# Kernel tuning notes

Measured on AMD Instinct MI355X. Metric: run time of the kernel, lower is better.

Reference implementation:

```python
import jax, jax.numpy as jnp
import numpy as np

H = 12        # heads
D = 768       # d_model
DK = D // H   # per-head dim
B, S = 1, 4096


def setup_inputs() -> dict:
    key = jax.random.key(0)
    ks = jax.random.split(key, 8)
    scale = 1.0 / np.sqrt(D)
    return {
        "q": jax.random.normal(ks[0], (B, S, D), jnp.float32),
        "k": jax.random.normal(ks[1], (B, S, D), jnp.float32),
        "v": jax.random.normal(ks[2], (B, S, D), jnp.float32),
        "Wq": jax.random.normal(ks[3], (D, D), jnp.float32) * scale,
        "bq": jnp.zeros((D,), jnp.float32),
        "Wk": jax.random.normal(ks[4], (D, D), jnp.float32) * scale,
        "bk": jnp.zeros((D,), jnp.float32),
        "Wv": jax.random.normal(ks[5], (D, D), jnp.float32) * scale,
        "bv": jnp.zeros((D,), jnp.float32),
        "Wo": jax.random.normal(ks[6], (D, D), jnp.float32) * scale,
        "bo": jnp.zeros((D,), jnp.float32),
    }


def reference(q, k, v, Wq, bq, Wk, bk, Wv, bv, Wo, bo):
    bs, sq, _ = q.shape
    sk = k.shape[1]
    # projections, then split heads: (b, h, s, dk)
    qh = (q @ Wq + bq).reshape(bs, sq, H, DK).transpose(0, 2, 1, 3)
    kh = (k @ Wk + bk).reshape(bs, sk, H, DK).transpose(0, 2, 1, 3)
    vh = (v @ Wv + bv).reshape(bs, sk, H, DK).transpose(0, 2, 1, 3)
    # scaled dot-product attention (mask=None, dropout inactive)
    scores = jnp.einsum("bhqd,bhkd->bhqk", qh, kh) / jnp.sqrt(jnp.float32(DK))
    attn = jax.nn.softmax(scores, axis=-1)
    ctx = jnp.einsum("bhqk,bhkd->bhqd", attn, vh)
    concat = ctx.transpose(0, 2, 1, 3).reshape(bs, sq, D)
    return concat @ Wo + bo
```

## Files before the change

kernel.cpp:

```cpp
#include <hip/hip_runtime.h>
#include <hip/hip_bf16.h>


constexpr int S_LEN = 4096;
constexpr int D_MODEL = 768;
constexpr int N_HEADS = 12;
constexpr int D_HEAD = 64;
constexpr int SEG = 2;
constexpr int SEG_LEN = S_LEN / SEG;
constexpr int NITER = SEG_LEN / 64;

#define QSCALE 0.180336880111120f

typedef _Float16 f16;
typedef __attribute__((ext_vector_type(8))) _Float16 f16x8;
typedef __attribute__((ext_vector_type(4))) _Float16 f16x4;
typedef __attribute__((ext_vector_type(4))) float f32x4;

__global__ __launch_bounds__(256) void prep_kernel(
    const float* __restrict__ q, const float* __restrict__ k,
    const float* __restrict__ v, f16* __restrict__ qh,
    f16* __restrict__ kh, f16* __restrict__ vh,
    const float* __restrict__ W0, const float* __restrict__ W1,
    const float* __restrict__ W2, const float* __restrict__ W3,
    f16* __restrict__ WtBase)
{
    __shared__ float T[64][65];
    int bid = blockIdx.x;
    const int t = threadIdx.x;
    if (bid < 4608) {
        int g = bid / 1536, r = bid % 1536;
        const float* x = (g == 0) ? q : (g == 1) ? k : v;
        f16* y = (g == 0) ? qh : (g == 1) ? kh : vh;
        int i = (r * 256 + t) * 8;
        float4 a = *(const float4*)&x[i];
        float4 b = *(const float4*)&x[i + 4];
        f16x8 h = { (f16)a.x, (f16)a.y, (f16)a.z, (f16)a.w,
                    (f16)b.x, (f16)b.y, (f16)b.z, (f16)b.w };
        *(f16x8*)&y[i] = h;
        return;
    }
    bid -= 4608;
    int g = bid / 144, r = bid % 144;
    const float* W = (g == 0) ? W0 : (g == 1) ? W1 : (g == 2) ? W2 : W3;
    f16* Wt = WtBase + (size_t)g * D_MODEL * D_MODEL;
    const int r0 = (r / 12) * 64;
    const int c0 = (r % 12) * 64;
    #pragma unroll
    for (int i = 0; i < 16; ++i) {
        int e = t + 256 * i; int rr = e >> 6, cc = e & 63;
        T[rr][cc] = W[(size_t)(r0 + rr) * D_MODEL + c0 + cc];
    }
    __syncthreads();
    #pragma unroll
    for (int i = 0; i < 16; ++i) {
        int e = t + 256 * i; int rr = e >> 6, cc = e & 63;
        Wt[(size_t)(c0 + rr) * D_MODEL + r0 + cc] = (f16)T[cc][rr];
    }
}

#define GSTR 72

__device__ __forceinline__ void gemm128_core(
    const f16* __restrict__ A, const f16* __restrict__ B,
    f16* As, f16* Bs, int K, int row0, int col0, int t, f32x4 acc[4][4])
{
    const int w = t >> 6, l = t & 63, quad = l >> 4, l15 = l & 15;
    const int wm = (w & 1) * 64, wn = (w >> 1) * 64;

    f16x8 pa[4], pb[4];
    #pragma unroll
    for (int i = 0; i < 4; ++i) {
        int idx = i * 256 + t;
        int r = idx >> 3, c = (idx & 7) * 8;
        pa[i] = *(const f16x8*)&A[(size_t)(row0 + r) * K + c];
        pb[i] = *(const f16x8*)&B[(size_t)(col0 + r) * K + c];
    }

    for (int k0 = 0; k0 < K; k0 += 64) {
        __syncthreads();
        #pragma unroll
        for (int i = 0; i < 4; ++i) {
            int idx = i * 256 + t;
            int r = idx >> 3, c = (idx & 7) * 8;
            *(f16x8*)&As[r * GSTR + c] = pa[i];
            *(f16x8*)&Bs[r * GSTR + c] = pb[i];
        }
        __syncthreads();

        int kn = k0 + 64;
        if (kn < K) {
            #pragma unroll
            for (int i = 0; i < 4; ++i) {
                int idx = i * 256 + t;
                int r = idx >> 3, c = (idx & 7) * 8;
                pa[i] = *(const f16x8*)&A[(size_t)(row0 + r) * K + kn + c];
                pb[i] = *(const f16x8*)&B[(size_t)(col0 + r) * K + kn + c];
            }
        }

        #pragma unroll
        for (int kc = 0; kc < 2; ++kc) {
            f16x8 af[4], bf[4];
            #pragma unroll
            for (int mt = 0; mt < 4; ++mt)
                af[mt] = *(f16x8*)&As[(wm + mt * 16 + l15) * GSTR + kc * 32 + quad * 8];
            #pragma unroll
            for (int nt = 0; nt < 4; ++nt)
                bf[nt] = *(f16x8*)&Bs[(wn + nt * 16 + l15) * GSTR + kc * 32 + quad * 8];
            #pragma unroll
            for (int mt = 0; mt < 4; ++mt)
                #pragma unroll
                for (int nt = 0; nt < 4; ++nt)
                    acc[mt][nt] = __builtin_amdgcn_mfma_f32_16x16x32_f16(
                        af[mt], bf[nt], acc[mt][nt], 0, 0, 0);
        }
    }
}

__global__ __launch_bounds__(256) void qkv_gemm_kernel(
    const f16* __restrict__ qh, const f16* __restrict__ kh,
    const f16* __restrict__ vh, const f16* __restrict__ WtBase,
    const float* __restrict__ bq, const float* __restrict__ bk,
    const float* __restrict__ bv,
    f16* __restrict__ Qp, f16* __restrict__ Kp, f16* __restrict__ Vpt)
{
    __shared__ f16 As[128 * GSTR];
    __shared__ f16 Bs[128 * GSTR];
    const size_t DD = (size_t)D_MODEL * D_MODEL;
    int bid = blockIdx.x;
    int g = bid / 192, r = bid % 192;

    const f16 *A, *B; const float* bias; f16* Y;
    int N; bool biasRow; float scale;
    int row0, col0;
    if (g == 0) {
        A = qh; B = WtBase; bias = bq; Y = Qp;
        N = D_MODEL; biasRow = false; scale = QSCALE;
        row0 = (r / 6) * 128; col0 = (r % 6) * 128;
    } else if (g == 1) {
        A = kh; B = WtBase + DD; bias = bk; Y = Kp;
        N = D_MODEL; biasRow = false; scale = 1.0f;
        row0 = (r / 6) * 128; col0 = (r % 6) * 128;
    } else {
        A = WtBase + 2 * DD; B = vh; bias = bv; Y = Vpt;
        N = S_LEN; biasRow = true; scale = 1.0f;
        row0 = (r / 32) * 128; col0 = (r % 32) * 128;
    }

    f32x4 acc[4][4];
    #pragma unroll
    for (int i = 0; i < 4; ++i)
        #pragma unroll
        for (int j = 0; j < 4; ++j) acc[i][j] = (f32x4){0.f, 0.f, 0.f, 0.f};

    const int t = threadIdx.x;
    gemm128_core(A, B, As, Bs, D_MODEL, row0, col0, t, acc);

    const int w = t >> 6, l = t & 63, quad = l >> 4, l15 = l & 15;
    const int wm = (w & 1) * 64, wn = (w >> 1) * 64;
    #pragma unroll
    for (int mt = 0; mt < 4; ++mt) {
        #pragma unroll
        for (int nt = 0; nt < 4; ++nt) {
            int col = col0 + wn + nt * 16 + l15;
            #pragma unroll
            for (int reg = 0; reg < 4; ++reg) {
                int row = row0 + wm + mt * 16 + quad * 4 + reg;
                float b = biasRow ? bias[row] : bias[col];
                Y[(size_t)row * N + col] = (f16)((acc[mt][nt][reg] + b) * scale);
            }
        }
    }
}

#define LSTR 72

__global__ __launch_bounds__(256, 4) void flash_attn_part_kernel(
    const f16* __restrict__ Q, const f16* __restrict__ K,
    const f16* __restrict__ Vg, f16* __restrict__ Opart,
    float* __restrict__ lsum)
{
    __shared__ f16 Ks[2][64 * LSTR];
    __shared__ f16 Vt[2][64 * LSTR];

    const int t    = threadIdx.x;
    const int w    = t >> 6;
    const int l    = t & 63;
    const int quad = l >> 4;
    const int l15  = l & 15;
    const int h    = blockIdx.y;
    const int q0   = blockIdx.x * 128;
    const int seg  = blockIdx.z;
    const int c0   = h * D_HEAD;
    const size_t SD = (size_t)S_LEN * D_MODEL;

    const int sr = t >> 3;
    const int sc = (t & 7) * 8;

    f16x8 qa[2][2];
    #pragma unroll
    for (int qt = 0; qt < 2; ++qt) {
        const f16* qrow = Q + (size_t)(q0 + w * 32 + qt * 16 + l15) * D_MODEL + c0;
        qa[qt][0] = *(const f16x8*)&qrow[quad * 8];
        qa[qt][1] = *(const f16x8*)&qrow[32 + quad * 8];
    }

    f32x4 ctx[2][4];
    float lAcc[2] = {0.f, 0.f};
    #pragma unroll
    for (int qt = 0; qt < 2; ++qt)
        #pragma unroll
        for (int i = 0; i < 4; ++i) ctx[qt][i] = (f32x4){0.f, 0.f, 0.f, 0.f};

    const int kt0 = seg * SEG_LEN;

    f16x8 kreg[2], vreg[2];
    #pragma unroll
    for (int i = 0; i < 2; ++i) {
        int r = i * 32 + sr;
        kreg[i] = *(const f16x8*)&K[(size_t)(kt0 + r) * D_MODEL + c0 + sc];
        vreg[i] = *(const f16x8*)&Vg[(size_t)(c0 + r) * S_LEN + kt0 + sc];
    }
    #pragma unroll
    for (int i = 0; i < 2; ++i) {
        int r = i * 32 + sr;
        *(f16x8*)&Ks[0][r * LSTR + sc] = kreg[i];
        *(f16x8*)&Vt[0][r * LSTR + sc] = vreg[i];
    }
    __syncthreads();
    #pragma unroll
    for (int i = 0; i < 2; ++i) {
        int r = i * 32 + sr;
        kreg[i] = *(const f16x8*)&K[(size_t)(kt0 + 64 + r) * D_MODEL + c0 + sc];
        vreg[i] = *(const f16x8*)&Vg[(size_t)(c0 + r) * S_LEN + kt0 + 64 + sc];
    }

    for (int it = 0; it < NITER; ++it) {
        const int buf = it & 1;
        const f16* ks = Ks[buf];
        const f16* vt = Vt[buf];

        f16x4 pfrag[2][4];
        #pragma unroll
        for (int nt = 0; nt < 4; ++nt) {
            f16x8 kb0 = *(const f16x8*)&ks[(nt * 16 + l15) * LSTR + quad * 8];
            f16x8 kb1 = *(const f16x8*)&ks[(nt * 16 + l15) * LSTR + 32 + quad * 8];
            #pragma unroll
            for (int qt = 0; qt < 2; ++qt) {
                f32x4 z = (f32x4){0.f, 0.f, 0.f, 0.f};
                z = __builtin_amdgcn_mfma_f32_16x16x32_f16(kb0, qa[qt][0], z, 0, 0, 0);
                z = __builtin_amdgcn_mfma_f32_16x16x32_f16(kb1, qa[qt][1], z, 0, 0, 0);
                float p0 = __builtin_amdgcn_exp2f(z[0]);
                float p1 = __builtin_amdgcn_exp2f(z[1]);
                float p2 = __builtin_amdgcn_exp2f(z[2]);
                float p3 = __builtin_amdgcn_exp2f(z[3]);
                lAcc[qt] += (p0 + p1) + (p2 + p3);
                pfrag[qt][nt] = (f16x4){ (f16)p0, (f16)p1, (f16)p2, (f16)p3 };
            }
        }
        #pragma unroll
        for (int mt = 0; mt < 4; ++mt) {
            #pragma unroll
            for (int nt = 0; nt < 4; ++nt) {
                f16x4 va = *(const f16x4*)&vt[(mt * 16 + l15) * LSTR + nt * 16 + quad * 4];
                #pragma unroll
                for (int qt = 0; qt < 2; ++qt)
                    ctx[qt][mt] = __builtin_amdgcn_mfma_f32_16x16x16f16(
                        va, pfrag[qt][nt], ctx[qt][mt], 0, 0, 0);
            }
        }

        if (it + 1 < NITER) {
            #pragma unroll
            for (int i = 0; i < 2; ++i) {
                int r = i * 32 + sr;
                *(f16x8*)&Ks[1 - buf][r * LSTR + sc] = kreg[i];
                *(f16x8*)&Vt[1 - buf][r * LSTR + sc] = vreg[i];
            }
        }
        __syncthreads();

        if (it + 2 < NITER) {
            int ktn = kt0 + (it + 2) * 64;
            #pragma unroll
            for (int i = 0; i < 2; ++i) {
                int r = i * 32 + sr;
                kreg[i] = *(const f16x8*)&K[(size_t)(ktn + r) * D_MODEL + c0 + sc];
                vreg[i] = *(const f16x8*)&Vg[(size_t)(c0 + r) * S_LEN + ktn + sc];
            }
        }
    }

    #pragma unroll
    for (int qt = 0; qt < 2; ++qt) {
        int qrow = q0 + w * 32 + qt * 16 + l15;
        #pragma unroll
        for (int mt = 0; mt < 4; ++mt) {
            f16x4 ov = { (f16)ctx[qt][mt][0], (f16)ctx[qt][mt][1],
                         (f16)ctx[qt][mt][2], (f16)ctx[qt][mt][3] };
            *(f16x4*)&Opart[(size_t)seg * SD + (size_t)qrow * D_MODEL
                            + c0 + mt * 16 + quad * 4] = ov;
        }
        float s = lAcc[qt];
        s += __shfl_xor(s, 16);
        s += __shfl_xor(s, 32);
        if (quad == 0)
            lsum[((size_t)seg * N_HEADS + h) * S_LEN + qrow] = s;
    }
}

__global__ __launch_bounds__(256) void combine_kernel(
    const f16* __restrict__ Opart, const float* __restrict__ lsum,
    f16* __restrict__ Ctx)
{
    const size_t SD = (size_t)S_LEN * D_MODEL;
    int tid = blockIdx.x * 256 + threadIdx.x;
    int idx = tid * 8;
    int row = idx / D_MODEL;
    int c   = idx % D_MODEL;
    int h   = c >> 6;
    float l0 = lsum[(size_t)h * S_LEN + row];
    float l1 = lsum[((size_t)N_HEADS + h) * S_LEN + row];
    float inv = 1.0f / (l0 + l1);
    f16x8 o0 = *(const f16x8*)&Opart[(size_t)row * D_MODEL + c];
    f16x8 o1 = *(const f16x8*)&Opart[SD + (size_t)row * D_MODEL + c];
    f16x8 r;
    #pragma unroll
    for (int j = 0; j < 8; ++j)
        r[j] = (f16)(((float)o0[j] + (float)o1[j]) * inv);
    *(f16x8*)&Ctx[(size_t)row * D_MODEL + c] = r;
}

__global__ __launch_bounds__(256) void oproj_kernel(
    const f16* __restrict__ Ctx, const f16* __restrict__ Wto,
    const float* __restrict__ bo, float* __restrict__ out)
{
    __shared__ f16 As[128 * GSTR];
    __shared__ f16 Bs[128 * GSTR];
    int bid = blockIdx.x;
    int row0 = (bid / 6) * 128, col0 = (bid % 6) * 128;

    f32x4 acc[4][4];
    #pragma unroll
    for (int i = 0; i < 4; ++i)
        #pragma unroll
        for (int j = 0; j < 4; ++j) acc[i][j] = (f32x4){0.f, 0.f, 0.f, 0.f};

    const int t = threadIdx.x;
    gemm128_core(Ctx, Wto, As, Bs, D_MODEL, row0, col0, t, acc);

    const int w = t >> 6, l = t & 63, quad = l >> 4, l15 = l & 15;
    const int wm = (w & 1) * 64, wn = (w >> 1) * 64;
    #pragma unroll
    for (int mt = 0; mt < 4; ++mt) {
        #pragma unroll
        for (int nt = 0; nt < 4; ++nt) {
            int col = col0 + wn + nt * 16 + l15;
            float b = bo[col];
            #pragma unroll
            for (int reg = 0; reg < 4; ++reg) {
                int row = row0 + wm + mt * 16 + quad * 4 + reg;
                out[(size_t)row * D_MODEL + col] = acc[mt][nt][reg] + b;
            }
        }
    }
}

extern "C" void kernel_launch(void* const* d_in, const int* in_sizes, int n_in,
                              void* d_out, int out_size, void* d_ws, size_t ws_size,
                              hipStream_t stream)
{
    const float* q  = (const float*)d_in[0];
    const float* k  = (const float*)d_in[1];
    const float* v  = (const float*)d_in[2];
    const float* Wq = (const float*)d_in[3];
    const float* bq = (const float*)d_in[4];
    const float* Wk = (const float*)d_in[5];
    const float* bk = (const float*)d_in[6];
    const float* Wv = (const float*)d_in[7];
    const float* bv = (const float*)d_in[8];
    const float* Wo = (const float*)d_in[9];
    const float* bo = (const float*)d_in[10];
    float* out = (float*)d_out;

    const size_t SD = (size_t)S_LEN * D_MODEL;
    const size_t DD = (size_t)D_MODEL * D_MODEL;
    f16* base   = (f16*)d_ws;
    f16* WtBase = base;
    f16* Wto    = WtBase + 3 * DD;
    f16* Qp     = base + 4 * DD;
    f16* Kp     = Qp + SD;
    f16* Vpt    = Kp + SD;
    f16* qh     = Vpt + SD;
    f16* kh     = qh + SD;
    f16* vh     = kh + SD;
    f16* Opart  = qh;
    f16* Ctx    = qh + 2 * SD;
    float* lsum = (float*)(base + 4 * DD + 6 * SD);

    prep_kernel<<<3 * 1536 + 4 * 144, 256, 0, stream>>>(
        q, k, v, qh, kh, vh, Wq, Wk, Wv, Wo, WtBase);

    qkv_gemm_kernel<<<3 * 192, 256, 0, stream>>>(
        qh, kh, vh, WtBase, bq, bk, bv, Qp, Kp, Vpt);

    dim3 gAttn(S_LEN / 128, N_HEADS, SEG);
    flash_attn_part_kernel<<<gAttn, 256, 0, stream>>>(Qp, Kp, Vpt, Opart, lsum);

    combine_kernel<<<1536, 256, 0, stream>>>(Opart, lsum, Ctx);

    oproj_kernel<<<192, 256, 0, stream>>>(Ctx, Wto, bo, out);
}
```

Before: 222.0 us.

## Use 512-thread attention blocks with one 16-row query tile per wave

Raises the flash-attention block from 4 to 8 waves, with each wave handling one 16-row query tile instead of two. Each thread now loads a single K/V staging row rather than two. This cuts per-thread register use and aims to raise occupancy (launch bounds 512,6). In exchange, each K/V tile in LDS is reused by fewer query rows per wave and there are more waves per barrier, which lowers MFMA work per LDS read and adds sync cost.

Measured after the change: 238.5 us. 1.07x slower.

```diff
diff --git a/kernel.cpp b/kernel.cpp
--- a/kernel.cpp
+++ b/kernel.cpp
@@ -176,7 +176,7 @@
 
 #define LSTR 72
 
-__global__ __launch_bounds__(256, 4) void flash_attn_part_kernel(
+__global__ __launch_bounds__(512, 6) void flash_attn_part_kernel(
     const f16* __restrict__ Q, const f16* __restrict__ K,
     const f16* __restrict__ Vg, f16* __restrict__ Opart,
     float* __restrict__ lsum)
@@ -198,115 +198,83 @@
     const int sr = t >> 3;
     const int sc = (t & 7) * 8;
 
-    f16x8 qa[2][2];
-    #pragma unroll
-    for (int qt = 0; qt < 2; ++qt) {
-        const f16* qrow = Q + (size_t)(q0 + w * 32 + qt * 16 + l15) * D_MODEL + c0;
-        qa[qt][0] = *(const f16x8*)&qrow[quad * 8];
-        qa[qt][1] = *(const f16x8*)&qrow[32 + quad * 8];
-    }
-
-    f32x4 ctx[2][4];
-    float lAcc[2] = {0.f, 0.f};
-    #pragma unroll
-    for (int qt = 0; qt < 2; ++qt)
-        #pragma unroll
-        for (int i = 0; i < 4; ++i) ctx[qt][i] = (f32x4){0.f, 0.f, 0.f, 0.f};
+    const f16* qrow = Q + (size_t)(q0 + w * 16 + l15) * D_MODEL + c0;
+    f16x8 qa0 = *(const f16x8*)&qrow[quad * 8];
+    f16x8 qa1 = *(const f16x8*)&qrow[32 + quad * 8];
+
+    f32x4 ctx[4];
+    float lAcc = 0.f;
+    #pragma unroll
+    for (int i = 0; i < 4; ++i) ctx[i] = (f32x4){0.f, 0.f, 0.f, 0.f};
 
     const int kt0 = seg * SEG_LEN;
 
-    f16x8 kreg[2], vreg[2];
-    #pragma unroll
-    for (int i = 0; i < 2; ++i) {
-        int r = i * 32 + sr;
-        kreg[i] = *(const f16x8*)&K[(size_t)(kt0 + r) * D_MODEL + c0 + sc];
-        vreg[i] = *(const f16x8*)&Vg[(size_t)(c0 + r) * S_LEN + kt0 + sc];
-    }
-    #pragma unroll
-    for (int i = 0; i < 2; ++i) {
-        int r = i * 32 + sr;
-        *(f16x8*)&Ks[0][r * LSTR + sc] = kreg[i];
-        *(f16x8*)&Vt[0][r * LSTR + sc] = vreg[i];
-    }
+    f16x8 kreg, vreg;
+    kreg = *(const f16x8*)&K[(size_t)(kt0 + sr) * D_MODEL + c0 + sc];
+    vreg = *(const f16x8*)&Vg[(size_t)(c0 + sr) * S_LEN + kt0 + sc];
+    *(f16x8*)&Ks[0][sr * LSTR + sc] = kreg;
+    *(f16x8*)&Vt[0][sr * LSTR + sc] = vreg;
     __syncthreads();
-    #pragma unroll
-    for (int i = 0; i < 2; ++i) {
-        int r = i * 32 + sr;
-        kreg[i] = *(const f16x8*)&K[(size_t)(kt0 + 64 + r) * D_MODEL + c0 + sc];
-        vreg[i] = *(const f16x8*)&Vg[(size_t)(c0 + r) * S_LEN + kt0 + 64 + sc];
-    }
+    kreg = *(const f16x8*)&K[(size_t)(kt0 + 64 + sr) * D_MODEL + c0 + sc];
+    vreg = *(const f16x8*)&Vg[(size_t)(c0 + sr) * S_LEN + kt0 + 64 + sc];
 
     for (int it = 0; it < NITER; ++it) {
         const int buf = it & 1;
         const f16* ks = Ks[buf];
         const f16* vt = Vt[buf];
 
-        f16x4 pfrag[2][4];
+        f16x4 pfrag[4];
         #pragma unroll
         for (int nt = 0; nt < 4; ++nt) {
             f16x8 kb0 = *(const f16x8*)&ks[(nt * 16 + l15) * LSTR + quad * 8];
             f16x8 kb1 = *(const f16x8*)&ks[(nt * 16 + l15) * LSTR + 32 + quad * 8];
-            #pragma unroll
-            for (int qt = 0; qt < 2; ++qt) {
-                f32x4 z = (f32x4){0.f, 0.f, 0.f, 0.f};
-                z = __builtin_amdgcn_mfma_f32_16x16x32_f16(kb0, qa[qt][0], z, 0, 0, 0);
-                z = __builtin_amdgcn_mfma_f32_16x16x32_f16(kb1, qa[qt][1], z, 0, 0, 0);
-                float p0 = __builtin_amdgcn_exp2f(z[0]);
-                float p1 = __builtin_amdgcn_exp2f(z[1]);
-                float p2 = __builtin_amdgcn_exp2f(z[2]);
-                float p3 = __builtin_amdgcn_exp2f(z[3]);
-                lAcc[qt] += (p0 + p1) + (p2 + p3);
-                pfrag[qt][nt] = (f16x4){ (f16)p0, (f16)p1, (f16)p2, (f16)p3 };
-            }
+            f32x4 z = (f32x4){0.f, 0.f, 0.f, 0.f};
+            z = __builtin_amdgcn_mfma_f32_16x16x32_f16(kb0, qa0, z, 0, 0, 0);
+            z = __builtin_amdgcn_mfma_f32_16x16x32_f16(kb1, qa1, z, 0, 0, 0);
+            float p0 = __builtin_amdgcn_exp2f(z[0]);
+            float p1 = __builtin_amdgcn_exp2f(z[1]);
+            float p2 = __builtin_amdgcn_exp2f(z[2]);
+            float p3 = __builtin_amdgcn_exp2f(z[3]);
+            lAcc += (p0 + p1) + (p2 + p3);
+            pfrag[nt] = (f16x4){ (f16)p0, (f16)p1, (f16)p2, (f16)p3 };
         }
         #pragma unroll
         for (int mt = 0; mt < 4; ++mt) {
             #pragma unroll
             for (int nt = 0; nt < 4; ++nt) {
                 f16x4 va = *(const f16x4*)&vt[(mt * 16 + l15) * LSTR + nt * 16 + quad * 4];
-                #pragma unroll
-                for (int qt = 0; qt < 2; ++qt)
-                    ctx[qt][mt] = __builtin_amdgcn_mfma_f32_16x16x16f16(
-                        va, pfrag[qt][nt], ctx[qt][mt], 0, 0, 0);
+                ctx[mt] = __builtin_amdgcn_mfma_f32_16x16x16f16(
+                    va, pfrag[nt], ctx[mt], 0, 0, 0);
             }
         }
 
         if (it + 1 < NITER) {
-            #pragma unroll
-            for (int i = 0; i < 2; ++i) {
-                int r = i * 32 + sr;
-                *(f16x8*)&Ks[1 - buf][r * LSTR + sc] = kreg[i];
-                *(f16x8*)&Vt[1 - buf][r * LSTR + sc] = vreg[i];
-            }
+            *(f16x8*)&Ks[1 - buf][sr * LSTR + sc] = kreg;
+            *(f16x8*)&Vt[1 - buf][sr * LSTR + sc] = vreg;
         }
         __syncthreads();
 
         if (it + 2 < NITER) {
             int ktn = kt0 + (it + 2) * 64;
-            #pragma unroll
-            for (int i = 0; i < 2; ++i) {
-                int r = i * 32 + sr;
-                kreg[i] = *(const f16x8*)&K[(size_t)(ktn + r) * D_MODEL + c0 + sc];
-                vreg[i] = *(const f16x8*)&Vg[(size_t)(c0 + r) * S_LEN + ktn + sc];
-            }
-        }
-    }
-
-    #pragma unroll
-    for (int qt = 0; qt < 2; ++qt) {
-        int qrow = q0 + w * 32 + qt * 16 + l15;
+            kreg = *(const f16x8*)&K[(size_t)(ktn + sr) * D_MODEL + c0 + sc];
+            vreg = *(const f16x8*)&Vg[(size_t)(c0 + sr) * S_LEN + ktn + sc];
+        }
+    }
+
+    {
+        int qrow_i = q0 + w * 16 + l15;
         #pragma unroll
         for (int mt = 0; mt < 4; ++mt) {
-            f16x4 ov = { (f16)ctx[qt][mt][0], (f16)ctx[qt][mt][1],
-                         (f16)ctx[qt][mt][2], (f16)ctx[qt][mt][3] };
-            *(f16x4*)&Opart[(size_t)seg * SD + (size_t)qrow * D_MODEL
+            f16x4 ov = { (f16)ctx[mt][0], (f16)ctx[mt][1],
+                         (f16)ctx[mt][2], (f16)ctx[mt][3] };
+            *(f16x4*)&Opart[(size_t)seg * SD + (size_t)qrow_i * D_MODEL
                             + c0 + mt * 16 + quad * 4] = ov;
         }
-        float s = lAcc[qt];
+        float s = lAcc;
         s += __shfl_xor(s, 16);
         s += __shfl_xor(s, 32);
         if (quad == 0)
-            lsum[((size_t)seg * N_HEADS + h) * S_LEN + qrow] = s;
+            lsum[((size_t)seg * N_HEADS + h) * S_LEN + qrow_i] = s;
     }
 }
 
@@ -406,7 +374,7 @@
         qh, kh, vh, WtBase, bq, bk, bv, Qp, Kp, Vpt);
 
     dim3 gAttn(S_LEN / 128, N_HEADS, SEG);
-    flash_attn_part_kernel<<<gAttn, 256, 0, stream>>>(Qp, Kp, Vpt, Opart, lsum);
+    flash_attn_part_kernel<<<gAttn, 512, 0, stream>>>(Qp, Kp, Vpt, Opart, lsum);
 
     combine_kernel<<<1536, 256, 0, stream>>>(Opart, lsum, Ctx);
 
```
